# Optimization experiments

Measured on AMD Instinct MI355X. Metric: run time of the kernel, lower is better.

The kernel has to match this reference:

```python
import jax, jax.numpy as jnp
import numpy as np
from jax import lax
from jax.scipy.stats import norm

KERNLEN = 31
NSIG = 4
EPS = 1e-3


def _gkern(kernlen=KERNLEN, nsig=NSIG):
    # Faithful port of HA._gkern (scipy.stats.norm.cdf -> jax.scipy.stats.norm.cdf)
    interval = (2.0 * nsig + 1.0) / kernlen
    x = jnp.linspace(-nsig - interval / 2.0, nsig + interval / 2.0, kernlen + 1)
    kern1d = jnp.diff(norm.cdf(x))
    kernel_raw = jnp.sqrt(jnp.outer(kern1d, kern1d))
    kernel = kernel_raw / kernel_raw.sum()
    return kernel.astype(jnp.float32)


def setup_inputs() -> dict:
    key = jax.random.key(0)
    attention = jax.random.uniform(key, (64, 1, 512, 512), dtype=jnp.float32)
    gaussian_kernel = _gkern()[None, None, :, :]  # OIHW [1,1,31,31]
    return {"attention": attention, "gaussian_kernel": gaussian_kernel}


def reference(attention, gaussian_kernel):
    a = jnp.clip(attention, 0.0, 1.0)
    # single-channel 31x31 conv, 'same' padding (pad 15)
    soft = lax.conv_general_dilated(
        a, gaussian_kernel,
        window_strides=(1, 1),
        padding=[(15, 15), (15, 15)],
        dimension_numbers=("NCHW", "OIHW", "NCHW"),
    )
    # per-image min-max normalization over H,W (per (n,c) slice)
    mx = soft.max(axis=(2, 3), keepdims=True)
    mn = soft.min(axis=(2, 3), keepdims=True)
    soft = (soft - mn) / jnp.maximum(mx - mn, EPS)  # torch.clamp(max-min, min=eps)
    soft = jnp.nan_to_num(soft, nan=0.0, posinf=1.0, neginf=0.0)
    return jnp.maximum(soft, a)
```

## Files before the change

### kernel.cpp

```cpp
#include <hip/hip_runtime.h>
#include <math.h>

#define IMGS 64
#define HWDIM 512
#define KLEN 31
#define RAD 15
#define EPSV 1e-3f
#define MM_STRIDE 32
#define ISTR 68


__global__ __launch_bounds__(128) void init_k(const float* __restrict__ gk,
                                              float* __restrict__ w,
                                              int* __restrict__ mm) {
    int t = threadIdx.x;
    if (t < KLEN) w[t] = sqrtf(gk[t * KLEN + t]);
    if (t < IMGS) { mm[t * MM_STRIDE] = 0x7F800000; mm[t * MM_STRIDE + 1] = 0; }
}

template <bool EDGE>
__device__ __forceinline__ void loadA(int i, const float* __restrict__ src,
                                      int x0, int y0, float4* __restrict__ b) {
    const int r = i >> 2, q = i & 3;
    int y = y0 - RAD + r;
    if (EDGE) y = y < 0 ? 0 : (y > HWDIM - 1 ? HWDIM - 1 : y);
    const float4* row = (const float4*)(src + ((size_t)y << 9));
    const int gb = (x0 >> 2) + (q << 2) - 4;
#pragma unroll
    for (int m = 0; m < 12; ++m) {
        int g = gb + m;
        if (EDGE) g = g < 0 ? 0 : (g > 127 ? 127 : g);
        b[m] = row[g];
    }
}

template <bool EDGE>
__device__ __forceinline__ void compA(int i, int x0, int y0,
                                      const float* __restrict__ wg,
                                      float* __restrict__ inter,
                                      const float4* __restrict__ b) {
    const int r = i >> 2, q = i & 3;
    const int y = y0 - RAD + r;
    const int gb = (x0 >> 2) + (q << 2) - 4;
    const bool vy = !EDGE || ((unsigned)y < HWDIM);
    float vv[48];
#pragma unroll
    for (int m = 0; m < 12; ++m) {
        const bool vx = !EDGE || (vy && ((unsigned)(gb + m) < 128u));
        vv[4 * m + 0] = vx ? fminf(fmaxf(b[m].x, 0.f), 1.f) : 0.f;
        vv[4 * m + 1] = vx ? fminf(fmaxf(b[m].y, 0.f), 1.f) : 0.f;
        vv[4 * m + 2] = vx ? fminf(fmaxf(b[m].z, 0.f), 1.f) : 0.f;
        vv[4 * m + 3] = vx ? fminf(fmaxf(b[m].w, 0.f), 1.f) : 0.f;
    }
    float* dst = &inter[r * ISTR + (q << 4)];
#pragma unroll
    for (int d = 0; d < 4; ++d) {
        float4 o;
        float* op = &o.x;
#pragma unroll
        for (int s = 0; s < 4; ++s) {
            const int oc = (d << 2) + s;
            float a = 0.f;
#pragma unroll
            for (int k = 0; k < KLEN; ++k) a += vv[oc + 1 + k] * wg[k];
            op[s] = a;
        }
        *(float4*)(dst + (d << 2)) = o;
    }
}

template <bool EDGE>
__device__ __forceinline__ void conv_body(const float* __restrict__ attn,
                                          float* __restrict__ out,
                                          const float* __restrict__ wg,
                                          int* __restrict__ mm,
                                          int img, int x0, int y0,
                                          float* __restrict__ inter,
                                          float* __restrict__ sred) {
    const int t = threadIdx.x;
    const float* src = attn + ((size_t)img << 18);

    {
        float4 bA[12], bB[12];
        const bool hasB = t < 120;
        loadA<EDGE>(t, src, x0, y0, bA);
        if (hasB) loadA<EDGE>(256 + t, src, x0, y0, bB);
        compA<EDGE>(t, x0, y0, wg, inter, bA);
        if (hasB) compA<EDGE>(256 + t, x0, y0, wg, inter, bB);
    }
    __syncthreads();

    const int tx = t & 15;
    const int ty = t >> 4;
    float4 acc[4];
#pragma unroll
    for (int i = 0; i < 4; ++i) acc[i] = make_float4(0.f, 0.f, 0.f, 0.f);
#pragma unroll
    for (int k = 0; k < 34; ++k) {
        const float4 v = *(const float4*)&inter[((ty << 2) + k) * ISTR + (tx << 2)];
#pragma unroll
        for (int i = 0; i < 4; ++i) {
            const int j = k - i;
            if (j >= 0 && j < KLEN) {
                const float w = wg[j];
                acc[i].x += v.x * w;
                acc[i].y += v.y * w;
                acc[i].z += v.z * w;
                acc[i].w += v.w * w;
            }
        }
    }
    float* dst = out + ((size_t)img << 18);
    float lmin = INFINITY, lmax = -INFINITY;
#pragma unroll
    for (int i = 0; i < 4; ++i) {
        *(float4*)&dst[(size_t)(y0 + (ty << 2) + i) * HWDIM + x0 + (tx << 2)] = acc[i];
        lmin = fminf(lmin, fminf(fminf(acc[i].x, acc[i].y), fminf(acc[i].z, acc[i].w)));
        lmax = fmaxf(lmax, fmaxf(fmaxf(acc[i].x, acc[i].y), fmaxf(acc[i].z, acc[i].w)));
    }
#pragma unroll
    for (int off = 1; off < 64; off <<= 1) {
        lmin = fminf(lmin, __shfl_xor(lmin, off, 64));
        lmax = fmaxf(lmax, __shfl_xor(lmax, off, 64));
    }
    const int lane = t & 63, wid = t >> 6;
    if (lane == 0) { sred[wid] = lmin; sred[4 + wid] = lmax; }
    __syncthreads();
    if (t == 0) {
        float bmin = fminf(fminf(sred[0], sred[1]), fminf(sred[2], sred[3]));
        float bmax = fmaxf(fmaxf(sred[4], sred[5]), fmaxf(sred[6], sred[7]));
        atomicMin(&mm[img * MM_STRIDE], __float_as_int(bmin));
        atomicMax(&mm[img * MM_STRIDE + 1], __float_as_int(bmax));
    }
}

__global__ __launch_bounds__(256, 2) void conv_k(const float* __restrict__ attn,
                                                 float* __restrict__ out,
                                                 const float* __restrict__ wg,
                                                 int* __restrict__ mm) {
    __shared__ float inter[94 * ISTR];
    __shared__ float sred[8];
    const int sw  = ((blockIdx.x & 7) << 9) + (blockIdx.x >> 3);
    const int img = sw >> 6;
    const int by  = (sw >> 3) & 7;
    const int bx  = sw & 7;
    const int x0 = bx << 6;
    const int y0 = by << 6;
    if (bx == 0 || bx == 7 || by == 0 || by == 7)
        conv_body<true>(attn, out, wg, mm, img, x0, y0, inter, sred);
    else
        conv_body<false>(attn, out, wg, mm, img, x0, y0, inter, sred);
}

__global__ __launch_bounds__(256) void final_k(const float* __restrict__ attn,
                                               float* __restrict__ out,
                                               const int* __restrict__ mm) {
    const int img = blockIdx.x >> 6;
    const float mn = __int_as_float(mm[img * MM_STRIDE]);
    const float mx = __int_as_float(mm[img * MM_STRIDE + 1]);
    const float inv = 1.0f / fmaxf(mx - mn, EPSV);
    const size_t base0 = ((size_t)blockIdx.x << 12) + ((size_t)threadIdx.x << 2);
#pragma unroll
    for (int h = 0; h < 4; ++h) {
        const size_t base = base0 + (size_t)h * 1024;
        float4 s = *(const float4*)(out + base);
        float4 a = *(const float4*)(attn + base);
        float4 o;
        o.x = fmaxf((s.x - mn) * inv, fminf(fmaxf(a.x, 0.f), 1.f));
        o.y = fmaxf((s.y - mn) * inv, fminf(fmaxf(a.y, 0.f), 1.f));
        o.z = fmaxf((s.z - mn) * inv, fminf(fmaxf(a.z, 0.f), 1.f));
        o.w = fmaxf((s.w - mn) * inv, fminf(fmaxf(a.w, 0.f), 1.f));
        *(float4*)(out + base) = o;
    }
}

extern "C" void kernel_launch(void* const* d_in, const int* in_sizes, int n_in,
                              void* d_out, int out_size, void* d_ws, size_t ws_size,
                              hipStream_t stream) {
    const float* attn = (const float*)d_in[0];
    const float* gk   = (const float*)d_in[1];
    float* out  = (float*)d_out;
    float* wsf  = (float*)d_ws;
    float* w1d  = wsf;
    int*   mm   = (int*)(wsf + 32);

    init_k<<<1, 128, 0, stream>>>(gk, w1d, mm);
    conv_k<<<4096, 256, 0, stream>>>(attn, out, w1d, mm);
    final_k<<<IMGS * HWDIM * HWDIM / 4096, 256, 0, stream>>>(attn, out, mm);
}
```

Baseline: 78.76 us.

## Halve conv tile height to 64x32 and remap horizontal-pass threads

The output tile per block shrinks from 64x64 to 64x32, so the grid doubles to 8192 blocks. Each thread now computes two output rows instead of four, and shared memory drops to 62 rows. The horizontal pass maps threads so each handles one of the 62 rows. The wave-serial second pass and the uneven two-phase horizontal load are removed. In exchange, the 30-row vertical halo is re-read and recomputed over fewer output rows, so redundant loads and horizontal FMAs per output rise, and 8 of 256 threads idle in the first phase.

```diff
diff --git a/kernel.cpp b/kernel.cpp
--- a/kernel.cpp
+++ b/kernel.cpp
@@ -19,57 +19,6 @@
 }
 
 template <bool EDGE>
-__device__ __forceinline__ void loadA(int i, const float* __restrict__ src,
-                                      int x0, int y0, float4* __restrict__ b) {
-    const int r = i >> 2, q = i & 3;
-    int y = y0 - RAD + r;
-    if (EDGE) y = y < 0 ? 0 : (y > HWDIM - 1 ? HWDIM - 1 : y);
-    const float4* row = (const float4*)(src + ((size_t)y << 9));
-    const int gb = (x0 >> 2) + (q << 2) - 4;
-#pragma unroll
-    for (int m = 0; m < 12; ++m) {
-        int g = gb + m;
-        if (EDGE) g = g < 0 ? 0 : (g > 127 ? 127 : g);
-        b[m] = row[g];
-    }
-}
-
-template <bool EDGE>
-__device__ __forceinline__ void compA(int i, int x0, int y0,
-                                      const float* __restrict__ wg,
-                                      float* __restrict__ inter,
-                                      const float4* __restrict__ b) {
-    const int r = i >> 2, q = i & 3;
-    const int y = y0 - RAD + r;
-    const int gb = (x0 >> 2) + (q << 2) - 4;
-    const bool vy = !EDGE || ((unsigned)y < HWDIM);
-    float vv[48];
-#pragma unroll
-    for (int m = 0; m < 12; ++m) {
-        const bool vx = !EDGE || (vy && ((unsigned)(gb + m) < 128u));
-        vv[4 * m + 0] = vx ? fminf(fmaxf(b[m].x, 0.f), 1.f) : 0.f;
-        vv[4 * m + 1] = vx ? fminf(fmaxf(b[m].y, 0.f), 1.f) : 0.f;
-        vv[4 * m + 2] = vx ? fminf(fmaxf(b[m].z, 0.f), 1.f) : 0.f;
-        vv[4 * m + 3] = vx ? fminf(fmaxf(b[m].w, 0.f), 1.f) : 0.f;
-    }
-    float* dst = &inter[r * ISTR + (q << 4)];
-#pragma unroll
-    for (int d = 0; d < 4; ++d) {
-        float4 o;
-        float* op = &o.x;
-#pragma unroll
-        for (int s = 0; s < 4; ++s) {
-            const int oc = (d << 2) + s;
-            float a = 0.f;
-#pragma unroll
-            for (int k = 0; k < KLEN; ++k) a += vv[oc + 1 + k] * wg[k];
-            op[s] = a;
-        }
-        *(float4*)(dst + (d << 2)) = o;
-    }
-}
-
-template <bool EDGE>
 __device__ __forceinline__ void conv_body(const float* __restrict__ attn,
                                           float* __restrict__ out,
                                           const float* __restrict__ wg,
@@ -81,25 +30,58 @@
     const float* src = attn + ((size_t)img << 18);
 
     {
-        float4 bA[12], bB[12];
-        const bool hasB = t < 120;
-        loadA<EDGE>(t, src, x0, y0, bA);
-        if (hasB) loadA<EDGE>(256 + t, src, x0, y0, bB);
-        compA<EDGE>(t, x0, y0, wg, inter, bA);
-        if (hasB) compA<EDGE>(256 + t, x0, y0, wg, inter, bB);
+        const int l = t & 7, q = (t >> 3) & 3, r = ((t >> 5) << 3) + l;
+        if (r < 62) {
+            int y = y0 - RAD + r;
+            if (EDGE) y = y < 0 ? 0 : (y > HWDIM - 1 ? HWDIM - 1 : y);
+            const float4* row = (const float4*)(src + ((size_t)y << 9));
+            const int gb = (x0 >> 2) + (q << 2) - 4;
+            float4 b[12];
+#pragma unroll
+            for (int m = 0; m < 12; ++m) {
+                int g = gb + m;
+                if (EDGE) g = g < 0 ? 0 : (g > 127 ? 127 : g);
+                b[m] = row[g];
+            }
+            const bool vy = !EDGE || ((unsigned)(y0 - RAD + r) < HWDIM);
+            float vv[48];
+#pragma unroll
+            for (int m = 0; m < 12; ++m) {
+                const bool vx = !EDGE || (vy && ((unsigned)(gb + m) < 128u));
+                vv[4 * m + 0] = vx ? fminf(fmaxf(b[m].x, 0.f), 1.f) : 0.f;
+                vv[4 * m + 1] = vx ? fminf(fmaxf(b[m].y, 0.f), 1.f) : 0.f;
+                vv[4 * m + 2] = vx ? fminf(fmaxf(b[m].z, 0.f), 1.f) : 0.f;
+                vv[4 * m + 3] = vx ? fminf(fmaxf(b[m].w, 0.f), 1.f) : 0.f;
+            }
+            float* dst = &inter[r * ISTR + (q << 4)];
+#pragma unroll
+            for (int d = 0; d < 4; ++d) {
+                float4 o;
+                float* op = &o.x;
+#pragma unroll
+                for (int s = 0; s < 4; ++s) {
+                    const int oc = (d << 2) + s;
+                    float a = 0.f;
+#pragma unroll
+                    for (int k = 0; k < KLEN; ++k) a += vv[oc + 1 + k] * wg[k];
+                    op[s] = a;
+                }
+                *(float4*)(dst + (d << 2)) = o;
+            }
+        }
     }
     __syncthreads();
 
     const int tx = t & 15;
     const int ty = t >> 4;
-    float4 acc[4];
+    float4 acc[2];
+    acc[0] = make_float4(0.f, 0.f, 0.f, 0.f);
+    acc[1] = make_float4(0.f, 0.f, 0.f, 0.f);
 #pragma unroll
-    for (int i = 0; i < 4; ++i) acc[i] = make_float4(0.f, 0.f, 0.f, 0.f);
+    for (int k = 0; k < 32; ++k) {
+        const float4 v = *(const float4*)&inter[((ty << 1) + k) * ISTR + (tx << 2)];
 #pragma unroll
-    for (int k = 0; k < 34; ++k) {
-        const float4 v = *(const float4*)&inter[((ty << 2) + k) * ISTR + (tx << 2)];
-#pragma unroll
-        for (int i = 0; i < 4; ++i) {
+        for (int i = 0; i < 2; ++i) {
             const int j = k - i;
             if (j >= 0 && j < KLEN) {
                 const float w = wg[j];
@@ -113,8 +95,8 @@
     float* dst = out + ((size_t)img << 18);
     float lmin = INFINITY, lmax = -INFINITY;
 #pragma unroll
-    for (int i = 0; i < 4; ++i) {
-        *(float4*)&dst[(size_t)(y0 + (ty << 2) + i) * HWDIM + x0 + (tx << 2)] = acc[i];
+    for (int i = 0; i < 2; ++i) {
+        *(float4*)&dst[(size_t)(y0 + (ty << 1) + i) * HWDIM + x0 + (tx << 2)] = acc[i];
         lmin = fminf(lmin, fminf(fminf(acc[i].x, acc[i].y), fminf(acc[i].z, acc[i].w)));
         lmax = fmaxf(lmax, fmaxf(fmaxf(acc[i].x, acc[i].y), fmaxf(acc[i].z, acc[i].w)));
     }
@@ -134,19 +116,19 @@
     }
 }
 
-__global__ __launch_bounds__(256, 2) void conv_k(const float* __restrict__ attn,
-                                                 float* __restrict__ out,
-                                                 const float* __restrict__ wg,
-                                                 int* __restrict__ mm) {
-    __shared__ float inter[94 * ISTR];
+__global__ __launch_bounds__(256) void conv_k(const float* __restrict__ attn,
+                                              float* __restrict__ out,
+                                              const float* __restrict__ wg,
+                                              int* __restrict__ mm) {
+    __shared__ float inter[62 * ISTR];
     __shared__ float sred[8];
-    const int sw  = ((blockIdx.x & 7) << 9) + (blockIdx.x >> 3);
-    const int img = sw >> 6;
-    const int by  = (sw >> 3) & 7;
+    const int sw  = ((blockIdx.x & 7) << 10) + (blockIdx.x >> 3);
+    const int img = sw >> 7;
+    const int by  = (sw >> 3) & 15;
     const int bx  = sw & 7;
     const int x0 = bx << 6;
-    const int y0 = by << 6;
-    if (bx == 0 || bx == 7 || by == 0 || by == 7)
+    const int y0 = by << 5;
+    if (bx == 0 || bx == 7 || by == 0 || by == 15)
         conv_body<true>(attn, out, wg, mm, img, x0, y0, inter, sred);
     else
         conv_body<false>(attn, out, wg, mm, img, x0, y0, inter, sred);
@@ -185,6 +167,6 @@
     int*   mm   = (int*)(wsf + 32);
 
     init_k<<<1, 128, 0, stream>>>(gk, w1d, mm);
-    conv_k<<<4096, 256, 0, stream>>>(attn, out, w1d, mm);
+    conv_k<<<8192, 256, 0, stream>>>(attn, out, w1d, mm);
     final_k<<<IMGS * HWDIM * HWDIM / 4096, 256, 0, stream>>>(attn, out, mm);
 }
```

Result: slower. 91.02 us (+15.6%).

## Remap horizontal-pass work items and use inline-asm loads with explicit waits

Applied to the files above, without the earlier changes.

The horizontal-pass thread-to-(row,quad) mapping is changed so each group of 8 lanes covers 8 consecutive rows for a given quad, with rows padded to 96 and dead lanes masking their stores. Global loads go through inline-asm dwordx4 instructions followed by a full vmcnt wait and sched barriers. The two work items per thread now run serially (load, wait, compute, then the second), where before both sets of loads were issued up front. This may cut load-issue overlap and add some dead lanes, in exchange for a different coalescing pattern.

```diff
diff --git a/kernel.cpp b/kernel.cpp
--- a/kernel.cpp
+++ b/kernel.cpp
@@ -9,6 +9,8 @@
 #define MM_STRIDE 32
 #define ISTR 68
 
+typedef float f32x4 __attribute__((ext_vector_type(4)));
+
 
 __global__ __launch_bounds__(128) void init_k(const float* __restrict__ gk,
                                               float* __restrict__ w,
@@ -18,31 +20,35 @@
     if (t < IMGS) { mm[t * MM_STRIDE] = 0x7F800000; mm[t * MM_STRIDE + 1] = 0; }
 }
 
+#define GLD(dst, ptr) \
+    asm volatile("global_load_dwordx4 %0, %1, off" : "=v"(dst) : "v"(ptr))
+
 template <bool EDGE>
-__device__ __forceinline__ void loadA(int i, const float* __restrict__ src,
-                                      int x0, int y0, float4* __restrict__ b) {
-    const int r = i >> 2, q = i & 3;
+__device__ __forceinline__ void itemA(int i, const float* __restrict__ src,
+                                      int x0, int y0,
+                                      const float* __restrict__ wg,
+                                      float* __restrict__ inter) {
+    const int rl = ((i >> 5) << 3) | (i & 7);
+    const bool live = rl < 94;
+    const int r = live ? rl : 93;
+    const int q = (i >> 3) & 3;
     int y = y0 - RAD + r;
     if (EDGE) y = y < 0 ? 0 : (y > HWDIM - 1 ? HWDIM - 1 : y);
-    const float4* row = (const float4*)(src + ((size_t)y << 9));
+    const float* row = src + ((size_t)y << 9);
     const int gb = (x0 >> 2) + (q << 2) - 4;
+
+    f32x4 b[12];
 #pragma unroll
     for (int m = 0; m < 12; ++m) {
         int g = gb + m;
         if (EDGE) g = g < 0 ? 0 : (g > 127 ? 127 : g);
-        b[m] = row[g];
+        GLD(b[m], row + (g << 2));
     }
-}
+    __builtin_amdgcn_sched_barrier(0);
+    asm volatile("s_waitcnt vmcnt(0)" ::: "memory");
+    __builtin_amdgcn_sched_barrier(0);
 
-template <bool EDGE>
-__device__ __forceinline__ void compA(int i, int x0, int y0,
-                                      const float* __restrict__ wg,
-                                      float* __restrict__ inter,
-                                      const float4* __restrict__ b) {
-    const int r = i >> 2, q = i & 3;
-    const int y = y0 - RAD + r;
-    const int gb = (x0 >> 2) + (q << 2) - 4;
-    const bool vy = !EDGE || ((unsigned)y < HWDIM);
+    const bool vy = !EDGE || ((unsigned)(y0 - RAD + r) < HWDIM);
     float vv[48];
 #pragma unroll
     for (int m = 0; m < 12; ++m) {
@@ -65,7 +71,7 @@
             for (int k = 0; k < KLEN; ++k) a += vv[oc + 1 + k] * wg[k];
             op[s] = a;
         }
-        *(float4*)(dst + (d << 2)) = o;
+        if (live) *(float4*)(dst + (d << 2)) = o;
     }
 }
 
@@ -80,14 +86,8 @@
     const int t = threadIdx.x;
     const float* src = attn + ((size_t)img << 18);
 
-    {
-        float4 bA[12], bB[12];
-        const bool hasB = t < 120;
-        loadA<EDGE>(t, src, x0, y0, bA);
-        if (hasB) loadA<EDGE>(256 + t, src, x0, y0, bB);
-        compA<EDGE>(t, x0, y0, wg, inter, bA);
-        if (hasB) compA<EDGE>(256 + t, x0, y0, wg, inter, bB);
-    }
+    itemA<EDGE>(t, src, x0, y0, wg, inter);
+    if (t < 128) itemA<EDGE>(256 + t, src, x0, y0, wg, inter);
     __syncthreads();
 
     const int tx = t & 15;
@@ -138,7 +138,7 @@
                                                  float* __restrict__ out,
                                                  const float* __restrict__ wg,
                                                  int* __restrict__ mm) {
-    __shared__ float inter[94 * ISTR];
+    __shared__ float inter[96 * ISTR];
     __shared__ float sred[8];
     const int sw  = ((blockIdx.x & 7) << 9) + (blockIdx.x >> 3);
     const int img = sw >> 6;
```

After: 82.84 us. 5.2% more time.
